# Kernel optimization log

Hardware: AMD Instinct MI355X
Metric: run time of the kernel (lower is better)

The kernel has to match this reference:

```python
import jax, jax.numpy as jnp
from jax import lax
import numpy as np

B, C, H, W = 4, 256, 128, 128
NC, NH = 19, 8
HD = C // NH
SCALE = HD ** -0.5
MOM = 0.1

def conv2d(x, w, b=None, pad=0, groups=1):
    y = lax.conv_general_dilated(x, w, (1, 1), [(pad, pad), (pad, pad)],
                                 dimension_numbers=('NCHW', 'OIHW', 'NCHW'),
                                 feature_group_count=groups)
    return y if b is None else y + b[None, :, None, None]

def layernorm(x, g, b, eps=1e-5):
    # LN over channel dim (original permutes to NHWC, LN, permutes back)
    mu = x.mean(1, keepdims=True)
    var = jnp.mean((x - mu) ** 2, 1, keepdims=True)
    return (x - mu) / jnp.sqrt(var + eps) * g[None, :, None, None] + b[None, :, None, None]

def setup_inputs():
    key = jax.random.key(0)
    ks = jax.random.split(key, 24)
    s = 0.02
    mem = jax.random.normal(ks[12], (1, NC, C), jnp.float32)
    mem = mem / jnp.linalg.norm(mem, axis=2, keepdims=True)  # F.normalize(dim=2)
    return dict(
        low=jax.random.normal(ks[0], (B, C, H, W), jnp.float32),
        high=jax.random.normal(ks[1], (B, C, H, W), jnp.float32),
        g_low=jnp.ones((C,), jnp.float32), b_low=jnp.zeros((C,), jnp.float32),
        g_high=jnp.ones((C,), jnp.float32), b_high=jnp.zeros((C,), jnp.float32),
        g_mlp=jnp.ones((C,), jnp.float32), b_mlp=jnp.zeros((C,), jnp.float32),
        w_q_dw=jax.random.normal(ks[2], (C, 1, 3, 3), jnp.float32) * s, b_q_dw=jnp.zeros((C,), jnp.float32),
        w_q_pw=jax.random.normal(ks[3], (C, C, 1, 1), jnp.float32) * s, b_q_pw=jnp.zeros((C,), jnp.float32),
        w_ml1=jax.random.normal(ks[4], (C, C // 4, 1, 1), jnp.float32) * s,
        w_ml2=jax.random.normal(ks[5], (NC, C, 1, 1), jnp.float32) * s,
        w_align=jax.random.normal(ks[6], (C, C // 4, 1, 1), jnp.float32) * s,
        w_kv=jax.random.normal(ks[7], (2 * C, C), jnp.float32) * s, b_kv=jnp.zeros((2 * C,), jnp.float32),
        memory=mem,
        w_proj=jax.random.normal(ks[8], (C, C, 1, 1), jnp.float32) * s, b_proj=jnp.zeros((C,), jnp.float32),
        w_mlp1=jax.random.normal(ks[9], (4 * C, C, 1, 1), jnp.float32) * s, b_mlp1=jnp.zeros((4 * C,), jnp.float32),
        w_mlp_dw=jax.random.normal(ks[10], (4 * C, 1, 3, 3), jnp.float32) * s, b_mlp_dw=jnp.zeros((4 * C,), jnp.float32),
        w_mlp2=jax.random.normal(ks[11], (C, 4 * C, 1, 1), jnp.float32) * s, b_mlp2=jnp.zeros((C,), jnp.float32),
    )

def _cpga(low, high, g_low, b_low, g_high, b_high, g_mlp, b_mlp,
          w_q_dw, b_q_dw, w_q_pw, b_q_pw, w_ml1, w_ml2, w_align,
          w_kv, b_kv, memory, w_proj, b_proj,
          w_mlp1, b_mlp1, w_mlp_dw, b_mlp_dw, w_mlp2, b_mlp2):
    query = layernorm(low, g_low, b_low)
    kv_in = layernorm(high, g_high, b_high)
    fused = (query + kv_in) * 0.5
    # CFEmbedding: learned class mask -> spatial softmax -> class prototypes
    mask = conv2d(conv2d(fused, w_ml1, groups=4), w_ml2)           # [B,NC,H,W]
    mask = jax.nn.softmax(mask.reshape(B, NC, H * W), axis=-1)
    xa = conv2d(fused, w_align, groups=4).reshape(B, C, H * W)
    cf = jnp.einsum('bnl,bcl->bnc', mask, xa)                      # [B,NC,C]
    cf = (1.0 - MOM) * cf + MOM * memory                           # memory mix (eval mode)
    kv = jnp.einsum('bnc,dc->bnd', cf, w_kv) + b_kv                # [B,NC,2C]
    k, v = jnp.split(kv, 2, axis=-1)                               # [B,NC,C] each
    # query path: depthwise-separable 3x3 conv
    q = conv2d(query, w_q_dw, b_q_dw, pad=1, groups=C)
    q = conv2d(q, w_q_pw, b_q_pw).reshape(B, NH, HD, H * W)        # [B,NH,HD,HW]
    kh = k.reshape(B, NC, NH, HD)
    vh = v.reshape(B, NC, NH, HD)
    attn = jnp.einsum('bhdl,bnhd->bhln', q, kh) * SCALE            # [B,NH,HW,NC]
    attn = jnp.max(attn, axis=-1, keepdims=True) - attn            # custom max-subtract
    attn = jax.nn.softmax(attn, axis=-1)
    out = jnp.einsum('bhln,bnhd->bhdl', attn, vh).reshape(B, C, H, W)
    out = conv2d(out, w_proj, b_proj) + low                        # residual 1
    # conv FFN: 1x1 expand -> depthwise 3x3 -> GELU -> 1x1 project
    y = layernorm(out, g_mlp, b_mlp)
    y = conv2d(y, w_mlp1, b_mlp1)
    y = conv2d(y, w_mlp_dw, b_mlp_dw, pad=1, groups=4 * C)
    y = jax.nn.gelu(y, approximate=False)
    y = conv2d(y, w_mlp2, b_mlp2)
    return out + y                                                 # residual 2

def reference(low, high, g_low, b_low, g_high, b_high, g_mlp, b_mlp,
              w_q_dw, b_q_dw, w_q_pw, b_q_pw, w_ml1, w_ml2, w_align,
              w_kv, b_kv, memory, w_proj, b_proj,
              w_mlp1, b_mlp1, w_mlp_dw, b_mlp_dw, w_mlp2, b_mlp2):
    return _cpga(low, high, g_low, b_low, g_high, b_high, g_mlp, b_mlp,
                 w_q_dw, b_q_dw, w_q_pw, b_q_pw, w_ml1, w_ml2, w_align,
                 w_kv, b_kv, memory, w_proj, b_proj,
                 w_mlp1, b_mlp1, w_mlp_dw, b_mlp_dw, w_mlp2, b_mlp2)
```

## Files before the change

### kernel.cpp

```cpp
#include <hip/hip_runtime.h>
#include <hip/hip_bf16.h>
#include <math.h>

using bf16 = __hip_bfloat16;
typedef __attribute__((ext_vector_type(8))) short bf16x8s;
typedef __attribute__((ext_vector_type(4))) float f32x4;

#define HWD 16384
#define CD 256
#define BD 4
#define NCD 19
#define SCALE_F 0.17677669529663687f

#define O_GLOW    0
#define O_BLOW    256
#define O_GHIGH   512
#define O_BHIGH   768
#define O_GMLP    1024
#define O_BMLP    1280
#define O_WQDW    1536
#define O_BQDW    3840
#define O_WQPW    4096
#define O_BQPW    69632
#define O_WML1    69888
#define O_WML2    86272
#define O_WALIGN  91136
#define O_WKV     107520
#define O_BKV     238592
#define O_MEM     239104
#define O_WPROJ   243968
#define O_BPROJ   309504
#define O_WMLP1   309760
#define O_BMLP1   571904
#define O_WMLPDW  572928
#define O_BMLPDW  582144
#define O_WMLP2   583168
#define O_BMLP2   845312
#define WTOTAL    845568

__device__ __forceinline__ float bfv(const bf16* p){ return __bfloat162float(*p); }
__device__ __forceinline__ float ldi(const void* p, size_t i, bool f32){
  return f32 ? ((const float*)p)[i] : __bfloat162float(((const bf16*)p)[i]);
}
__device__ __forceinline__ void sto(void* p, size_t i, float v, bool f32){
  if (f32) ((float*)p)[i] = v; else ((bf16*)p)[i] = __float2bfloat16(v);
}

__device__ __forceinline__ void gld16(const bf16* g, bf16* l){
  __builtin_amdgcn_global_load_lds(
      (const __attribute__((address_space(1))) unsigned int*)g,
      (__attribute__((address_space(3))) unsigned int*)l, 16, 0, 0);
}

__global__ void detect_kernel(const unsigned* __restrict__ g, int* __restrict__ flag){
  if (threadIdx.x == 0) *flag = (g[0] == 0x3F800000u) ? 1 : 0;
}

struct WSrc { const void* p[24]; };
__global__ __launch_bounds__(256) void convert_kernel(WSrc a, bf16* __restrict__ WB,
                                                      const int* __restrict__ flag){
  const bool fin = *flag != 0;
  const int SZ[24] = {256,256,256,256,256,256, 2304,256, 65536,256,
                      16384,4864,16384, 131072,512,4864, 65536,256,
                      262144,1024, 9216,1024, 262144,256};
  size_t i = (size_t)blockIdx.x*256 + threadIdx.x;
  if (i >= WTOTAL) return;
  size_t base = 0; int seg = 0; size_t loc = 0;
  #pragma unroll
  for (int s = 0; s < 24; s++){
    if (i >= base && i < base + (size_t)SZ[s]){ seg = s; loc = i - base; }
    base += (size_t)SZ[s];
  }
  WB[i] = __float2bfloat16(ldi(a.p[seg], loc, fin));
}

#define TSWZ(row, c) ((c) ^ (((row) >> 2) << 3))

__global__ __launch_bounds__(256) void ln_fuse_kernel(
    const void* __restrict__ low, const void* __restrict__ high,
    const bf16* __restrict__ WB, bf16* __restrict__ Q, bf16* __restrict__ F,
    const int* __restrict__ flag){
  const bool fin = *flag != 0;
  union SMU { float red[16][64][4]; bf16 tile[64][256]; };
  __shared__ SMU sm;
  __shared__ float stats[4][64];
  int t = threadIdx.x;
  int pq = t & 15, cs = t >> 4;
  int lg0 = blockIdx.x * 64;
  int b = lg0 >> 14, ll0 = lg0 & (HWD-1);
  size_t pbase = (size_t)b*CD*HWD + (size_t)ll0 + pq*4;
  int c0 = cs*16;

  float s1[4]={0,0,0,0}, s2[4]={0,0,0,0}, u1[4]={0,0,0,0}, u2[4]={0,0,0,0};
  for (int k=0;k<16;k++){
    size_t off = pbase + (size_t)(c0+k)*HWD;
    float xl[4], xh[4];
    if (fin){
      float4 a = *(const float4*)((const float*)low + off);
      float4 h = *(const float4*)((const float*)high + off);
      xl[0]=a.x; xl[1]=a.y; xl[2]=a.z; xl[3]=a.w;
      xh[0]=h.x; xh[1]=h.y; xh[2]=h.z; xh[3]=h.w;
    } else {
      ushort4 a = *(const ushort4*)((const bf16*)low + off);
      ushort4 h = *(const ushort4*)((const bf16*)high + off);
      const bf16* ap=(const bf16*)&a; const bf16* hp=(const bf16*)&h;
      #pragma unroll
      for (int q=0;q<4;q++){ xl[q]=__bfloat162float(ap[q]); xh[q]=__bfloat162float(hp[q]); }
    }
    #pragma unroll
    for (int q=0;q<4;q++){
      s1[q]+=xl[q]; s2[q]+=xl[q]*xl[q];
      u1[q]+=xh[q]; u2[q]+=xh[q]*xh[q];
    }
  }
  #pragma unroll
  for (int q=0;q<4;q++){
    sm.red[cs][pq*4+q][0]=s1[q]; sm.red[cs][pq*4+q][1]=s2[q];
    sm.red[cs][pq*4+q][2]=u1[q]; sm.red[cs][pq*4+q][3]=u2[q];
  }
  __syncthreads();
  if (t < 64){
    float a=0.f,b2=0.f,c=0.f,d=0.f;
    #pragma unroll
    for (int j=0;j<16;j++){
      a+=sm.red[j][t][0]; b2+=sm.red[j][t][1];
      c+=sm.red[j][t][2]; d+=sm.red[j][t][3];
    }
    float ml=a*(1.f/CD), vl=b2*(1.f/CD)-ml*ml;
    float mh=c*(1.f/CD), vh=d*(1.f/CD)-mh*mh;
    stats[0][t]=ml; stats[1][t]=rsqrtf(vl+1e-5f);
    stats[2][t]=mh; stats[3][t]=rsqrtf(vh+1e-5f);
  }
  __syncthreads();
  float mlq[4],rlq[4],mhq[4],rhq[4];
  #pragma unroll
  for (int q=0;q<4;q++){
    mlq[q]=stats[0][pq*4+q]; rlq[q]=stats[1][pq*4+q];
    mhq[q]=stats[2][pq*4+q]; rhq[q]=stats[3][pq*4+q];
  }

  for (int k=0;k<16;k++){
    int c = c0+k;
    size_t off = pbase + (size_t)c*HWD;
    float xl[4];
    if (fin){
      float4 a = *(const float4*)((const float*)low + off);
      xl[0]=a.x; xl[1]=a.y; xl[2]=a.z; xl[3]=a.w;
    } else {
      ushort4 a = *(const ushort4*)((const bf16*)low + off);
      const bf16* ap=(const bf16*)&a;
      #pragma unroll
      for (int q=0;q<4;q++) xl[q]=__bfloat162float(ap[q]);
    }
    float g = bfv(WB+O_GLOW+c), bb = bfv(WB+O_BLOW+c);
    #pragma unroll
    for (int q=0;q<4;q++){
      int row = pq*4+q;
      sm.tile[row][TSWZ(row, c)] = __float2bfloat16((xl[q]-mlq[q])*rlq[q]*g + bb);
    }
  }
  __syncthreads();
  {
    bf16* qb = Q + (size_t)lg0*CD;
    #pragma unroll
    for (int it=0; it<8; it++){
      int idx = it*256 + t;
      int row = idx >> 5, col = (idx & 31)*8;
      *(uint4*)(qb + (size_t)idx*8) = *(const uint4*)(&sm.tile[row][TSWZ(row, col)]);
    }
  }
  __syncthreads();

  for (int k=0;k<16;k++){
    int c = c0+k;
    size_t off = pbase + (size_t)c*HWD;
    float xl[4], xh[4];
    if (fin){
      float4 a = *(const float4*)((const float*)low + off);
      float4 h = *(const float4*)((const float*)high + off);
      xl[0]=a.x; xl[1]=a.y; xl[2]=a.z; xl[3]=a.w;
      xh[0]=h.x; xh[1]=h.y; xh[2]=h.z; xh[3]=h.w;
    } else {
      ushort4 a = *(const ushort4*)((const bf16*)low + off);
      ushort4 h = *(const ushort4*)((const bf16*)high + off);
      const bf16* ap=(const bf16*)&a; const bf16* hp=(const bf16*)&h;
      #pragma unroll
      for (int q=0;q<4;q++){ xl[q]=__bfloat162float(ap[q]); xh[q]=__bfloat162float(hp[q]); }
    }
    float gl = bfv(WB+O_GLOW+c),  bl = bfv(WB+O_BLOW+c);
    float gh = bfv(WB+O_GHIGH+c), bh = bfv(WB+O_BHIGH+c);
    #pragma unroll
    for (int q=0;q<4;q++){
      int row = pq*4+q;
      float qv = (xl[q]-mlq[q])*rlq[q]*gl + bl;
      float hv = (xh[q]-mhq[q])*rhq[q]*gh + bh;
      sm.tile[row][TSWZ(row, c)] = __float2bfloat16(0.5f*(qv+hv));
    }
  }
  __syncthreads();
  {
    bf16* fb = F + (size_t)lg0*CD;
    #pragma unroll
    for (int it=0; it<8; it++){
      int idx = it*256 + t;
      int row = idx >> 5, col = (idx & 31)*8;
      *(uint4*)(fb + (size_t)idx*8) = *(const uint4*)(&sm.tile[row][TSWZ(row, col)]);
    }
  }
}

__global__ __launch_bounds__(256) void ln_kernel(
    const bf16* __restrict__ x, const bf16* __restrict__ WB, bf16* __restrict__ out){
  int lg = blockIdx.x*256 + threadIdx.x;
  const bf16* xr = x + (size_t)lg*CD;
  float s1=0.f, s2=0.f;
  for (int v8=0; v8<32; v8++){
    uint4 vv = *(const uint4*)(xr + v8*8);
    const bf16* bb = (const bf16*)&vv;
    #pragma unroll
    for (int i=0;i<8;i++){ float x0 = __bfloat162float(bb[i]); s1+=x0; s2+=x0*x0; }
  }
  float m = s1*(1.f/CD), v = s2*(1.f/CD)-m*m, r = rsqrtf(v+1e-5f);
  bf16* orr = out + (size_t)lg*CD;
  for (int v8=0; v8<32; v8++){
    uint4 vv = *(const uint4*)(xr + v8*8);
    const bf16* bb = (const bf16*)&vv;
    #pragma unroll
    for (int i=0;i<8;i++){
      int c = v8*8+i;
      orr[c] = __float2bfloat16((__bfloat162float(bb[i])-m)*r*bfv(WB+O_GMLP+c) + bfv(WB+O_BMLP+c));
    }
  }
}

template<int LT, int K, bool GROUPED, int OUTMODE, int RESMODE, bool HASBIAS, bool SWAP>
__global__ __launch_bounds__(256) void gemm_kernel(
    const bf16* __restrict__ X, int xstride,
    const bf16* __restrict__ W, const bf16* __restrict__ bias,
    const void* __restrict__ resv, void* __restrict__ outv,
    int ostride, int co_limit, int out_off, const int* __restrict__ flag){
  constexpr int IF = LT/64;
  constexpr int NI = SWAP ? 4 : IF;
  constexpr int NJ = SWAP ? IF : 4;
  __shared__ bf16 As[64*32];
  __shared__ bf16 Bs[LT*32];
  int t = threadIdx.x, w = t>>6, lane = t&63;
  int l0 = blockIdx.x*LT;
  int co0 = blockIdx.y*64;
  int koff = GROUPED ? co0 : 0;
  f32x4 acc[4][4];
  #pragma unroll
  for (int i=0;i<4;i++)
    #pragma unroll
    for (int j=0;j<4;j++) acc[i][j] = (f32x4){0.f,0.f,0.f,0.f};

  int sub = lane>>2, kp = lane&3;
  int a_co = co0 + w*16 + sub; if (a_co >= co_limit) a_co = co_limit-1;
  const bf16* aW = W + (size_t)a_co*K + kp*8;
  const bf16* bRow = X + (size_t)(l0 + w*(LT/4) + sub)*xstride + koff + kp*8;
  bf16* aL = As + w*512;
  int frow = lane & 15, fk = (lane>>4)*8;
  const bf16* xrd = Bs + ((w*(LT/4) + frow)*32 + fk);
  const bf16* wrd = As + (frow*32 + fk);

  for (int k0 = 0; k0 < K; k0 += 32){
    __syncthreads();
    gld16(aW + k0, aL);
    #pragma unroll
    for (int j=0;j<IF;j++)
      gld16(bRow + (size_t)j*16*xstride + k0, Bs + (size_t)(w*IF+j)*512);
    __syncthreads();
    bf16x8s xf[IF], wf[4];
    #pragma unroll
    for (int i=0;i<IF;i++) xf[i] = *(const bf16x8s*)(xrd + i*512);
    #pragma unroll
    for (int i=0;i<4;i++)  wf[i] = *(const bf16x8s*)(wrd + i*512);
    #pragma unroll
    for (int i=0;i<NI;i++)
      #pragma unroll
      for (int j=0;j<NJ;j++)
        acc[i][j] = SWAP
          ? __builtin_amdgcn_mfma_f32_16x16x32_bf16(wf[i], xf[j], acc[i][j], 0,0,0)
          : __builtin_amdgcn_mfma_f32_16x16x32_bf16(xf[i], wf[j], acc[i][j], 0,0,0);
  }

  const bool fio = *flag != 0;
  #pragma unroll
  for (int i=0;i<NI;i++){
    #pragma unroll
    for (int j=0;j<NJ;j++){
      #pragma unroll
      for (int r=0;r<4;r++){
        int l, co;
        if (SWAP){ co = co0 + i*16 + (lane>>4)*4 + r; l = l0 + w*(LT/4) + j*16 + (lane&15); }
        else     { l = l0 + w*(LT/4) + i*16 + (lane>>4)*4 + r; co = co0 + j*16 + (lane&15); }
        float v = acc[i][j][r];
        if (HASBIAS) v += __bfloat162float(bias[co]);
        if (RESMODE==2){
          int b = l>>14, ll = l & (HWD-1);
          v += ldi(resv, ((size_t)(b*CD+co))*HWD + ll, fio);
        }
        if (RESMODE==1) v += __bfloat162float(((const bf16*)resv)[(size_t)l*CD + co]);
        if (OUTMODE==0) ((bf16*)outv)[(size_t)l*ostride + co] = __float2bfloat16(v);
        else if (OUTMODE==1){ if (co < co_limit) ((float*)outv)[(size_t)l*ostride + co] = v; }
        else sto(outv, (size_t)out_off + (size_t)co*HWD + l, v, fio);
      }
    }
  }
}

template<int CH, bool GELU>
__global__ __launch_bounds__(256) void dw3x3_kernel(
    const bf16* __restrict__ x, const bf16* __restrict__ w,
    const bf16* __restrict__ bias, bf16* __restrict__ out){
  constexpr int CPG = CH/8;
  constexpr int PPI = 256/CPG;
  constexpr int PPB = PPI*8;
  int t = threadIdx.x;
  int cg = t % CPG, pr = t / CPG;
  int c0 = cg*8;
  float wv[8][9], bv[8];
  #pragma unroll
  for (int i=0;i<8;i++){
    bv[i] = __bfloat162float(bias[c0+i]);
    #pragma unroll
    for (int k=0;k<9;k++) wv[i][k] = __bfloat162float(w[(c0+i)*9+k]);
  }
  int p0 = blockIdx.x * PPB;
  for (int it=0; it<8; it++){
    int px = p0 + it*PPI + pr;
    int l = px & (HWD-1);
    int y = l >> 7, xx = l & 127;
    float acc[8];
    #pragma unroll
    for (int i=0;i<8;i++) acc[i] = bv[i];
    #pragma unroll
    for (int dy=-1;dy<=1;dy++){
      int yy = y+dy; if ((unsigned)yy >= 128u) continue;
      #pragma unroll
      for (int dx=-1;dx<=1;dx++){
        int x2 = xx+dx; if ((unsigned)x2 >= 128u) continue;
        const bf16* pp = x + ((size_t)px + dy*128 + dx)*CH + c0;
        uint4 vv = *(const uint4*)pp;
        const bf16* bb = (const bf16*)&vv;
        #pragma unroll
        for (int i=0;i<8;i++) acc[i] += wv[i][(dy+1)*3+dx+1]*__bfloat162float(bb[i]);
      }
    }
    bf16* orow = out + (size_t)px*CH + c0;
    #pragma unroll
    for (int i=0;i<8;i++){
      float v = acc[i];
      if (GELU) v = 0.5f*v*(1.f+erff(v*0.70710678118f));
      orow[i] = __float2bfloat16(v);
    }
  }
}

__global__ __launch_bounds__(256) void pmax_kernel(const float* __restrict__ M, float* __restrict__ PMX){
  int b = blockIdx.y, tile = blockIdx.x, t = threadIdx.x;
  float mx[NCD];
  #pragma unroll
  for (int n=0;n<NCD;n++) mx[n] = -1e30f;
  for (int p = t; p < 512; p += 256){
    const float* r = M + ((size_t)b*HWD + tile*512 + p)*NCD;
    #pragma unroll
    for (int n=0;n<NCD;n++) mx[n] = fmaxf(mx[n], r[n]);
  }
  int lane = t&63, wv = t>>6;
  __shared__ float red[4][NCD];
  #pragma unroll
  for (int n=0;n<NCD;n++){
    float v = mx[n];
    for (int o=32;o;o>>=1) v = fmaxf(v, __shfl_down(v,o));
    if (lane==0) red[wv][n] = v;
  }
  __syncthreads();
  if (t < NCD)
    PMX[(b*32+tile)*NCD + t] = fmaxf(fmaxf(red[0][t],red[1][t]), fmaxf(red[2][t],red[3][t]));
}

__global__ void fmax_kernel(const float* __restrict__ PMX, float* __restrict__ MX, float* __restrict__ DEN){
  int t = threadIdx.x;
  if (t < BD*NCD){
    int b = t / NCD, n = t % NCD;
    float v = -1e30f;
    for (int i=0;i<32;i++) v = fmaxf(v, PMX[(b*32+i)*NCD + n]);
    MX[t] = v; DEN[t] = 0.f;
  }
}

__global__ __launch_bounds__(256) void exp_kernel(float* __restrict__ M,
    const float* __restrict__ MX, float* __restrict__ DEN){
  int b = blockIdx.y, t = threadIdx.x;
  float* r = M + ((size_t)b*HWD + blockIdx.x*256 + t)*NCD;
  float den[NCD];
  #pragma unroll
  for (int n=0;n<NCD;n++){ float e = expf(r[n] - MX[b*NCD+n]); r[n] = e; den[n] = e; }
  int lane = t&63, wv = t>>6;
  __shared__ float red[4][NCD];
  #pragma unroll
  for (int n=0;n<NCD;n++){
    float v = den[n];
    for (int o=32;o;o>>=1) v += __shfl_down(v,o);
    if (lane==0) red[wv][n] = v;
  }
  __syncthreads();
  if (t < NCD) atomicAdd(&DEN[b*NCD+t], red[0][t]+red[1][t]+red[2][t]+red[3][t]);
}

__global__ __launch_bounds__(256) void cfp_kernel(const float* __restrict__ M,
    const bf16* __restrict__ xa, float* __restrict__ PCF){
  int b = blockIdx.y, lt = blockIdx.x, c = threadIdx.x;
  float acc[NCD];
  #pragma unroll
  for (int n=0;n<NCD;n++) acc[n] = 0.f;
  for (int p=0;p<256;p++){
    size_t l = (size_t)b*HWD + lt*256 + p;
    float xv = __bfloat162float(xa[l*CD + c]);
    const float* e = M + l*NCD;
    #pragma unroll
    for (int n=0;n<NCD;n++) acc[n] += e[n]*xv;
  }
  float* o = PCF + ((size_t)(b*64+lt)*NCD)*CD + c;
  #pragma unroll
  for (int n=0;n<NCD;n++) o[n*CD] = acc[n];
}

__global__ __launch_bounds__(256) void cfr_kernel(const float* __restrict__ PCF,
    const float* __restrict__ DEN, float* __restrict__ CF){
  int idx = blockIdx.x*256 + threadIdx.x;
  if (idx >= BD*NCD*CD) return;
  int c = idx & 255, bn = idx >> 8;
  int b = bn / NCD, n = bn % NCD;
  float s = 0.f;
  for (int lt=0; lt<64; lt++) s += PCF[((size_t)(b*64+lt)*NCD + n)*CD + c];
  CF[(size_t)bn*CD + c] = s / DEN[b*NCD+n];
}

__global__ __launch_bounds__(256) void kv_kernel(const float* __restrict__ CF,
    const bf16* __restrict__ WB, float* __restrict__ KV){
  int idx = blockIdx.x*256 + threadIdx.x;
  if (idx >= BD*NCD*512) return;
  int d = idx & 511, bn = idx >> 9;
  int n = bn % NCD;
  float acc = bfv(WB + O_BKV + d);
  const float* cfr = CF + (size_t)bn*CD;
  const bf16* mr = WB + O_MEM + n*CD;
  const bf16* wr = WB + O_WKV + (size_t)d*CD;
  for (int c=0;c<CD;c++)
    acc += (0.9f*cfr[c] + 0.1f*bfv(mr+c)) * bfv(wr+c);
  KV[(size_t)bn*512 + d] = acc;
}

__global__ __launch_bounds__(256) void attn_kernel(const bf16* __restrict__ q,
    const float* __restrict__ KV, bf16* __restrict__ out){
  __shared__ float ks[NCD][256], vs[NCD][256];
  int t = threadIdx.x;
  int b = blockIdx.y, lt = blockIdx.x;
  for (int i=t; i<NCD*512; i+=256){
    int n = i>>9, d = i&511;
    float v = KV[(size_t)(b*NCD+n)*512 + d];
    if (d < 256) ks[n][d] = v; else vs[n][d-256] = v;
  }
  __syncthreads();
  int p = t & 31, h = t >> 5;
  size_t lg = (size_t)b*HWD + lt*32 + p;
  const bf16* qr = q + lg*CD + h*32;
  float qd[32];
  #pragma unroll
  for (int v8=0; v8<4; v8++){
    uint4 vv = *(const uint4*)(qr + v8*8);
    const bf16* bb = (const bf16*)&vv;
    #pragma unroll
    for (int i=0;i<8;i++) qd[v8*8+i] = __bfloat162float(bb[i]);
  }
  float s[NCD];
  #pragma unroll
  for (int n=0;n<NCD;n++){
    const float* kr = &ks[n][h*32];
    float a = 0.f;
    #pragma unroll
    for (int d=0;d<32;d++) a += qd[d]*kr[d];
    s[n] = a * SCALE_F;
  }
  float mn = s[0];
  #pragma unroll
  for (int n=1;n<NCD;n++) mn = fminf(mn, s[n]);
  float sum = 0.f;
  #pragma unroll
  for (int n=0;n<NCD;n++){ s[n] = expf(mn - s[n]); sum += s[n]; }
  float inv = 1.f/sum;
  bf16* orow = out + lg*CD + h*32;
  #pragma unroll
  for (int d=0;d<32;d++){
    float o = 0.f;
    #pragma unroll
    for (int n=0;n<NCD;n++) o += s[n]*vs[n][h*32+d];
    orow[d] = __float2bfloat16(o*inv);
  }
}

extern "C" void kernel_launch(void* const* d_in, const int* in_sizes, int n_in,
                              void* d_out, int out_size, void* d_ws, size_t ws_size,
                              hipStream_t stream){
  const void* low  = d_in[0];
  const void* high = d_in[1];

  char* ws = (char*)d_ws;
  bf16* B1 = (bf16*)(ws);
  bf16* B2 = (bf16*)(ws + ((size_t)32<<20));
  bf16* B3 = (bf16*)(ws + ((size_t)64<<20));
  bf16* B4 = (bf16*)(ws + ((size_t)96<<20));
  float* M  = (float*)(ws + ((size_t)128<<20));
  float* PCF= (float*)(ws + ((size_t)134<<20));
  bf16* WB  = (bf16*)(ws + ((size_t)140<<20));
  float* PMX= (float*)(ws + ((size_t)142<<20));
  float* MX = (float*)(ws + ((size_t)142<<20) + (64<<10));
  float* DEN= (float*)(ws + ((size_t)142<<20) + (80<<10));
  float* CF = (float*)(ws + ((size_t)142<<20) + (96<<10));
  float* KV = (float*)(ws + ((size_t)142<<20) + (256<<10));
  int* FLAG = (int*)  (ws + ((size_t)142<<20) + (512<<10));

  dim3 blk(256);

  detect_kernel<<<1, 64, 0, stream>>>((const unsigned*)d_in[2], FLAG);

  WSrc src;
  for (int i=0;i<24;i++) src.p[i] = d_in[i+2];
  convert_kernel<<<(WTOTAL+255)/256, blk, 0, stream>>>(src, WB, FLAG);

  ln_fuse_kernel<<<1024, blk, 0, stream>>>(low, high, WB, B1, B2, FLAG);
  gemm_kernel<256,64,true,0,0,false,false><<<dim3(256,4), blk, 0, stream>>>(
      B2, 256, WB+O_WML1, nullptr, nullptr, B3, 256, 256, 0, FLAG);
  gemm_kernel<128,256,false,1,0,false,false><<<dim3(512,1), blk, 0, stream>>>(
      B3, 256, WB+O_WML2, nullptr, nullptr, M, NCD, NCD, 0, FLAG);
  pmax_kernel<<<dim3(32,BD), blk, 0, stream>>>(M, PMX);
  fmax_kernel<<<1, 128, 0, stream>>>(PMX, MX, DEN);
  exp_kernel<<<dim3(64,BD), blk, 0, stream>>>(M, MX, DEN);
  gemm_kernel<256,64,true,0,0,false,false><<<dim3(256,4), blk, 0, stream>>>(
      B2, 256, WB+O_WALIGN, nullptr, nullptr, B3, 256, 256, 0, FLAG);
  cfp_kernel<<<dim3(64,BD), blk, 0, stream>>>(M, B3, PCF);
  cfr_kernel<<<(BD*NCD*CD+255)/256, blk, 0, stream>>>(PCF, DEN, CF);
  kv_kernel<<<(BD*NCD*512+255)/256, blk, 0, stream>>>(CF, WB, KV);
  dw3x3_kernel<256,false><<<1024, blk, 0, stream>>>(B1, WB+O_WQDW, WB+O_BQDW, B2);
  gemm_kernel<256,256,false,0,0,true,false><<<dim3(256,4), blk, 0, stream>>>(
      B2, 256, WB+O_WQPW, WB+O_BQPW, nullptr, B3, 256, 256, 0, FLAG);
  attn_kernel<<<dim3(512,BD), blk, 0, stream>>>(B3, KV, B2);
  gemm_kernel<256,256,false,0,2,true,false><<<dim3(256,4), blk, 0, stream>>>(
      B2, 256, WB+O_WPROJ, WB+O_BPROJ, low, B1, 256, 256, 0, FLAG);
  ln_kernel<<<256, blk, 0, stream>>>(B1, WB, B2);
  for (int b = 0; b < BD; b++){
    gemm_kernel<256,256,false,0,0,true,false><<<dim3(64,16), blk, 0, stream>>>(
        B2 + (size_t)b*HWD*CD, 256, WB+O_WMLP1, WB+O_BMLP1, nullptr, B3, 1024, 1024, 0, FLAG);
    dw3x3_kernel<1024,true><<<1024, blk, 0, stream>>>(B3, WB+O_WMLPDW, WB+O_BMLPDW, B4);
    gemm_kernel<128,1024,false,2,1,true,true><<<dim3(128,4), blk, 0, stream>>>(
        B4, 1024, WB+O_WMLP2, WB+O_BMLP2, B1 + (size_t)b*HWD*CD, d_out, 0, 256, b*CD*HWD, FLAG);
  }
}
```

Before: 909.6 us.

## Raise parallelism in layernorm, depthwise conv and class-feature partials

The LN kernel moves from one thread per row to four threads per row, holding the row in registers, combining partial sums with shuffles and writing vector stores. It launches 4x more blocks, and the row is no longer read twice. The depthwise conv kernels take an iteration-count template parameter and launch twice as many blocks with half the work each. The cfp partial reduction splits into 128 tiles instead of 64, and its partial buffer moves into the B4 region. The ln_fuse kernel writes its F output before Q, which may keep the low/high reads warmer in cache. The cost is more blocks and a larger partial buffer for cfr to reduce, and the reused B4 region must not overlap live data.

```diff
diff --git a/kernel.cpp b/kernel.cpp
--- a/kernel.cpp
+++ b/kernel.cpp
@@ -142,38 +142,6 @@
   for (int k=0;k<16;k++){
     int c = c0+k;
     size_t off = pbase + (size_t)c*HWD;
-    float xl[4];
-    if (fin){
-      float4 a = *(const float4*)((const float*)low + off);
-      xl[0]=a.x; xl[1]=a.y; xl[2]=a.z; xl[3]=a.w;
-    } else {
-      ushort4 a = *(const ushort4*)((const bf16*)low + off);
-      const bf16* ap=(const bf16*)&a;
-      #pragma unroll
-      for (int q=0;q<4;q++) xl[q]=__bfloat162float(ap[q]);
-    }
-    float g = bfv(WB+O_GLOW+c), bb = bfv(WB+O_BLOW+c);
-    #pragma unroll
-    for (int q=0;q<4;q++){
-      int row = pq*4+q;
-      sm.tile[row][TSWZ(row, c)] = __float2bfloat16((xl[q]-mlq[q])*rlq[q]*g + bb);
-    }
-  }
-  __syncthreads();
-  {
-    bf16* qb = Q + (size_t)lg0*CD;
-    #pragma unroll
-    for (int it=0; it<8; it++){
-      int idx = it*256 + t;
-      int row = idx >> 5, col = (idx & 31)*8;
-      *(uint4*)(qb + (size_t)idx*8) = *(const uint4*)(&sm.tile[row][TSWZ(row, col)]);
-    }
-  }
-  __syncthreads();
-
-  for (int k=0;k<16;k++){
-    int c = c0+k;
-    size_t off = pbase + (size_t)c*HWD;
     float xl[4], xh[4];
     if (fin){
       float4 a = *(const float4*)((const float*)low + off);
@@ -207,29 +175,71 @@
       *(uint4*)(fb + (size_t)idx*8) = *(const uint4*)(&sm.tile[row][TSWZ(row, col)]);
     }
   }
+  __syncthreads();
+
+  for (int k=0;k<16;k++){
+    int c = c0+k;
+    size_t off = pbase + (size_t)c*HWD;
+    float xl[4];
+    if (fin){
+      float4 a = *(const float4*)((const float*)low + off);
+      xl[0]=a.x; xl[1]=a.y; xl[2]=a.z; xl[3]=a.w;
+    } else {
+      ushort4 a = *(const ushort4*)((const bf16*)low + off);
+      const bf16* ap=(const bf16*)&a;
+      #pragma unroll
+      for (int q=0;q<4;q++) xl[q]=__bfloat162float(ap[q]);
+    }
+    float g = bfv(WB+O_GLOW+c), bb = bfv(WB+O_BLOW+c);
+    #pragma unroll
+    for (int q=0;q<4;q++){
+      int row = pq*4+q;
+      sm.tile[row][TSWZ(row, c)] = __float2bfloat16((xl[q]-mlq[q])*rlq[q]*g + bb);
+    }
+  }
+  __syncthreads();
+  {
+    bf16* qb = Q + (size_t)lg0*CD;
+    #pragma unroll
+    for (int it=0; it<8; it++){
+      int idx = it*256 + t;
+      int row = idx >> 5, col = (idx & 31)*8;
+      *(uint4*)(qb + (size_t)idx*8) = *(const uint4*)(&sm.tile[row][TSWZ(row, col)]);
+    }
+  }
 }
 
 __global__ __launch_bounds__(256) void ln_kernel(
     const bf16* __restrict__ x, const bf16* __restrict__ WB, bf16* __restrict__ out){
-  int lg = blockIdx.x*256 + threadIdx.x;
-  const bf16* xr = x + (size_t)lg*CD;
+  int t = threadIdx.x;
+  int rb = t >> 2, part = t & 3;
+  int lg = blockIdx.x*64 + rb;
+  int cb = part*64;
+  const bf16* xr = x + (size_t)lg*CD + cb;
+  uint4 v[8];
   float s1=0.f, s2=0.f;
-  for (int v8=0; v8<32; v8++){
-    uint4 vv = *(const uint4*)(xr + v8*8);
-    const bf16* bb = (const bf16*)&vv;
-    #pragma unroll
-    for (int i=0;i<8;i++){ float x0 = __bfloat162float(bb[i]); s1+=x0; s2+=x0*x0; }
-  }
-  float m = s1*(1.f/CD), v = s2*(1.f/CD)-m*m, r = rsqrtf(v+1e-5f);
-  bf16* orr = out + (size_t)lg*CD;
-  for (int v8=0; v8<32; v8++){
-    uint4 vv = *(const uint4*)(xr + v8*8);
-    const bf16* bb = (const bf16*)&vv;
-    #pragma unroll
-    for (int i=0;i<8;i++){
-      int c = v8*8+i;
-      orr[c] = __float2bfloat16((__bfloat162float(bb[i])-m)*r*bfv(WB+O_GMLP+c) + bfv(WB+O_BMLP+c));
-    }
+  #pragma unroll
+  for (int i=0;i<8;i++){
+    v[i] = *(const uint4*)(xr + i*8);
+    const bf16* bb = (const bf16*)&v[i];
+    #pragma unroll
+    for (int j=0;j<8;j++){ float x0 = __bfloat162float(bb[j]); s1+=x0; s2+=x0*x0; }
+  }
+  s1 += __shfl_xor(s1,1); s1 += __shfl_xor(s1,2);
+  s2 += __shfl_xor(s2,1); s2 += __shfl_xor(s2,2);
+  float m = s1*(1.f/CD), var = s2*(1.f/CD)-m*m, r = rsqrtf(var+1e-5f);
+  bf16* orr = out + (size_t)lg*CD + cb;
+  #pragma unroll
+  for (int i=0;i<8;i++){
+    uint4 o;
+    const bf16* bb = (const bf16*)&v[i];
+    bf16* ob = (bf16*)&o;
+    #pragma unroll
+    for (int j=0;j<8;j++){
+      int c = cb + i*8 + j;
+      ob[j] = __float2bfloat16((__bfloat162float(bb[j])-m)*r*bfv(WB+O_GMLP+c) + bfv(WB+O_BMLP+c));
+    }
+    *(uint4*)(orr + i*8) = o;
   }
 }
 
@@ -309,13 +319,13 @@
   }
 }
 
-template<int CH, bool GELU>
+template<int CH, bool GELU, int IT>
 __global__ __launch_bounds__(256) void dw3x3_kernel(
     const bf16* __restrict__ x, const bf16* __restrict__ w,
     const bf16* __restrict__ bias, bf16* __restrict__ out){
   constexpr int CPG = CH/8;
   constexpr int PPI = 256/CPG;
-  constexpr int PPB = PPI*8;
+  constexpr int PPB = PPI*IT;
   int t = threadIdx.x;
   int cg = t % CPG, pr = t / CPG;
   int c0 = cg*8;
@@ -327,7 +337,7 @@
     for (int k=0;k<9;k++) wv[i][k] = __bfloat162float(w[(c0+i)*9+k]);
   }
   int p0 = blockIdx.x * PPB;
-  for (int it=0; it<8; it++){
+  for (int it=0; it<IT; it++){
     int px = p0 + it*PPI + pr;
     int l = px & (HWD-1);
     int y = l >> 7, xx = l & 127;
@@ -415,14 +425,14 @@
   float acc[NCD];
   #pragma unroll
   for (int n=0;n<NCD;n++) acc[n] = 0.f;
-  for (int p=0;p<256;p++){
-    size_t l = (size_t)b*HWD + lt*256 + p;
+  for (int p=0;p<128;p++){
+    size_t l = (size_t)b*HWD + lt*128 + p;
     float xv = __bfloat162float(xa[l*CD + c]);
     const float* e = M + l*NCD;
     #pragma unroll
     for (int n=0;n<NCD;n++) acc[n] += e[n]*xv;
   }
-  float* o = PCF + ((size_t)(b*64+lt)*NCD)*CD + c;
+  float* o = PCF + ((size_t)(b*128+lt)*NCD)*CD + c;
   #pragma unroll
   for (int n=0;n<NCD;n++) o[n*CD] = acc[n];
 }
@@ -434,7 +444,7 @@
   int c = idx & 255, bn = idx >> 8;
   int b = bn / NCD, n = bn % NCD;
   float s = 0.f;
-  for (int lt=0; lt<64; lt++) s += PCF[((size_t)(b*64+lt)*NCD + n)*CD + c];
+  for (int lt=0; lt<128; lt++) s += PCF[((size_t)(b*128+lt)*NCD + n)*CD + c];
   CF[(size_t)bn*CD + c] = s / DEN[b*NCD+n];
 }
 
@@ -513,7 +523,7 @@
   bf16* B3 = (bf16*)(ws + ((size_t)64<<20));
   bf16* B4 = (bf16*)(ws + ((size_t)96<<20));
   float* M  = (float*)(ws + ((size_t)128<<20));
-  float* PCF= (float*)(ws + ((size_t)134<<20));
+  float* PCF= (float*)(ws + ((size_t)96<<20));
   bf16* WB  = (bf16*)(ws + ((size_t)140<<20));
   float* PMX= (float*)(ws + ((size_t)142<<20));
   float* MX = (float*)(ws + ((size_t)142<<20) + (64<<10));
@@ -540,20 +550,20 @@
   exp_kernel<<<dim3(64,BD), blk, 0, stream>>>(M, MX, DEN);
   gemm_kernel<256,64,true,0,0,false,false><<<dim3(256,4), blk, 0, stream>>>(
       B2, 256, WB+O_WALIGN, nullptr, nullptr, B3, 256, 256, 0, FLAG);
-  cfp_kernel<<<dim3(64,BD), blk, 0, stream>>>(M, B3, PCF);
+  cfp_kernel<<<dim3(128,BD), blk, 0, stream>>>(M, B3, PCF);
   cfr_kernel<<<(BD*NCD*CD+255)/256, blk, 0, stream>>>(PCF, DEN, CF);
   kv_kernel<<<(BD*NCD*512+255)/256, blk, 0, stream>>>(CF, WB, KV);
-  dw3x3_kernel<256,false><<<1024, blk, 0, stream>>>(B1, WB+O_WQDW, WB+O_BQDW, B2);
+  dw3x3_kernel<256,false,4><<<2048, blk, 0, stream>>>(B1, WB+O_WQDW, WB+O_BQDW, B2);
   gemm_kernel<256,256,false,0,0,true,false><<<dim3(256,4), blk, 0, stream>>>(
       B2, 256, WB+O_WQPW, WB+O_BQPW, nullptr, B3, 256, 256, 0, FLAG);
   attn_kernel<<<dim3(512,BD), blk, 0, stream>>>(B3, KV, B2);
   gemm_kernel<256,256,false,0,2,true,false><<<dim3(256,4), blk, 0, stream>>>(
       B2, 256, WB+O_WPROJ, WB+O_BPROJ, low, B1, 256, 256, 0, FLAG);
-  ln_kernel<<<256, blk, 0, stream>>>(B1, WB, B2);
+  ln_kernel<<<1024, blk, 0, stream>>>(B1, WB, B2);
   for (int b = 0; b < BD; b++){
     gemm_kernel<256,256,false,0,0,true,false><<<dim3(64,16), blk, 0, stream>>>(
         B2 + (size_t)b*HWD*CD, 256, WB+O_WMLP1, WB+O_BMLP1, nullptr, B3, 1024, 1024, 0, FLAG);
-    dw3x3_kernel<1024,true><<<1024, blk, 0, stream>>>(B3, WB+O_WMLPDW, WB+O_BMLPDW, B4);
+    dw3x3_kernel<1024,true,4><<<2048, blk, 0, stream>>>(B3, WB+O_WMLPDW, WB+O_BMLPDW, B4);
     gemm_kernel<128,1024,false,2,1,true,true><<<dim3(128,4), blk, 0, stream>>>(
         B4, 1024, WB+O_WMLP2, WB+O_BMLP2, B1 + (size_t)b*HWD*CD, d_out, 0, 256, b*CD*HWD, FLAG);
   }
```

New measurement: 908.2 us. About the same (-0.2%).
